# Kernel optimization log

Hardware: AMD Instinct MI355X
Metric: run time of the kernel (lower is better)

Reference implementation:

```python
import jax, jax.numpy as jnp
import numpy as np

B, L, H = 2, 2048, 2048
DI, N, DTR, K = 4096, 16, 128, 4  # intermediate, state, dt_rank, conv kernel


def setup_inputs() -> dict:
    key = jax.random.key(0)
    ks = jax.random.split(key, 8)
    x = jax.random.normal(ks[0], (B, L, H), jnp.float32)
    in_proj_w = jax.random.normal(ks[1], (2 * DI, H), jnp.float32) * 0.02
    conv1d_w = jax.random.normal(ks[2], (DI, 1, K), jnp.float32) * 0.1
    conv1d_b = jnp.zeros((DI,), jnp.float32)
    x_proj_w = jax.random.normal(ks[3], (DTR + 2 * N, DI), jnp.float32) * 0.02
    bound = DTR ** -0.5
    dt_proj_w = jax.random.uniform(ks[4], (DI, DTR), jnp.float32, -bound, bound)
    # faithful dt bias init: inverse-softplus of dt ~ Uniform-log[0.001, 0.1]
    dt = jnp.exp(jax.random.uniform(ks[5], (DI,), jnp.float32)
                 * (np.log(0.1) - np.log(0.001)) + np.log(0.001))
    dt = jnp.clip(dt, 1e-4)
    dt_proj_b = dt + jnp.log(-jnp.expm1(-dt))
    A_log = jnp.log(jnp.broadcast_to(jnp.arange(1, N + 1, dtype=jnp.float32), (DI, N)))
    D = jnp.ones((DI,), jnp.float32)
    out_proj_w = jax.random.normal(ks[6], (H, DI), jnp.float32) * 0.02
    return dict(x=x, in_proj_w=in_proj_w, conv1d_w=conv1d_w, conv1d_b=conv1d_b,
                x_proj_w=x_proj_w, dt_proj_w=dt_proj_w, dt_proj_b=dt_proj_b,
                A_log=A_log, D=D, out_proj_w=out_proj_w)


def _mamba_forward(x, in_proj_w, conv1d_w, conv1d_b, x_proj_w,
                   dt_proj_w, dt_proj_b, A_log, D, out_proj_w):
    # in_proj -> split into ssm input and gate (res)
    x_and_res = jnp.einsum('blh,eh->ble', x, in_proj_w)          # [B,L,2*DI]
    xi, res = jnp.split(x_and_res, 2, axis=-1)                    # [B,L,DI] each

    # depthwise causal conv1d (kernel K, left-pad K-1, truncated to L)
    xc = jnp.transpose(xi, (0, 2, 1))                             # [B,DI,L]
    xc = jax.lax.conv_general_dilated(
        xc, conv1d_w, window_strides=(1,), padding=((K - 1, 0),),
        dimension_numbers=('NCH', 'OIH', 'NCH'), feature_group_count=DI)
    xc = xc + conv1d_b[None, :, None]
    u = jax.nn.silu(jnp.transpose(xc, (0, 2, 1)))                 # [B,L,DI]

    # selective SSM parameters
    A = -jnp.exp(A_log.astype(jnp.float32))                       # [DI,N]
    x_dbl = jnp.einsum('bld,ed->ble', u, x_proj_w)                # [B,L,DTR+2N]
    dlt, Bm, Cm = jnp.split(x_dbl, [DTR, DTR + N], axis=-1)
    delta = jax.nn.softplus(jnp.einsum('blr,dr->bld', dlt, dt_proj_w) + dt_proj_b)

    # selective scan over time; carry h: [B,DI,N]
    def step(h, inp):
        d_t, B_t, C_t, u_t = inp                                  # [B,DI],[B,N],[B,N],[B,DI]
        dA = jnp.exp(d_t[:, :, None] * A)                         # [B,DI,N]
        h = dA * h + d_t[:, :, None] * B_t[:, None, :] * u_t[:, :, None]
        y_t = jnp.einsum('bdn,bn->bd', h, C_t)
        return h, y_t

    xs = (jnp.transpose(delta, (1, 0, 2)), jnp.transpose(Bm, (1, 0, 2)),
          jnp.transpose(Cm, (1, 0, 2)), jnp.transpose(u, (1, 0, 2)))
    h0 = jnp.zeros((x.shape[0], DI, N), jnp.float32)
    _, ys = jax.lax.scan(step, h0, xs)                            # ys: [L,B,DI]
    y = jnp.transpose(ys, (1, 0, 2)) + u * D.astype(jnp.float32)  # skip via D

    y = y * jax.nn.silu(res)                                      # gate
    return jnp.einsum('bld,hd->blh', y, out_proj_w)               # [B,L,H]


def reference(x, in_proj_w, conv1d_w, conv1d_b, x_proj_w,
              dt_proj_w, dt_proj_b, A_log, D, out_proj_w):
    return _mamba_forward(x, in_proj_w, conv1d_w, conv1d_b, x_proj_w,
                          dt_proj_w, dt_proj_b, A_log, D, out_proj_w)
```

## Files before the change

kernel.cpp:

```cpp
#include <hip/hip_runtime.h>
#include <hip/hip_bf16.h>
#include <stdint.h>

#define DEV static __device__ __forceinline__

typedef __attribute__((ext_vector_type(8))) short short8;
typedef __attribute__((ext_vector_type(4))) float f32x4;
typedef __attribute__((address_space(3))) void lds_void;
typedef __attribute__((address_space(1))) void glb_void;

constexpr int CB = 2, CL = 2048, CH = 2048, CDI = 4096, CN = 16, CDTR = 128;
constexpr int BLR = CB * CL;
constexpr int NC = 32, LC = 64;

DEV ushort f2b(float f) {
  union { float f; uint32_t u; } v; v.f = f;
  uint32_t u = v.u;
  return (ushort)((u + 0x7fffu + ((u >> 16) & 1u)) >> 16);
}
DEV float b2f(ushort b) {
  union { uint32_t u; float f; } v; v.u = ((uint32_t)b) << 16;
  return v.f;
}
DEV void gload16(const ushort* g, ushort* l) {
  __builtin_amdgcn_global_load_lds((const glb_void*)g, (lds_void*)l, 16, 0, 0);
}

__global__ void cast_kernel(const float* __restrict__ in, ushort* __restrict__ out, int n4) {
  int i = blockIdx.x * blockDim.x + threadIdx.x;
  if (i >= n4) return;
  float4 v = *(const float4*)(in + (size_t)i * 4);
  *(ushort4*)(out + (size_t)i * 4) = make_ushort4(f2b(v.x), f2b(v.y), f2b(v.z), f2b(v.w));
}

__global__ void cast_pad_xproj_kernel(const float* __restrict__ in, ushort* __restrict__ out) {
  int i = blockIdx.x * blockDim.x + threadIdx.x;
  if (i >= (256 * 4096 / 4)) return;
  int idx = i * 4;
  int r = idx >> 12;
  ushort4 o;
  if (r < 160) {
    float4 v = *(const float4*)(in + idx);
    o = make_ushort4(f2b(v.x), f2b(v.y), f2b(v.z), f2b(v.w));
  } else {
    o = make_ushort4(0, 0, 0, 0);
  }
  *(ushort4*)(out + idx) = o;
}

__global__ void dlt_cast_kernel(const float* __restrict__ xdbl, ushort* __restrict__ dlt) {
  int i = blockIdx.x * blockDim.x + threadIdx.x;
  if (i >= (BLR * CDTR / 4)) return;
  int idx = i * 4;
  int m = idx >> 7, c = idx & 127;
  float4 v = *(const float4*)(xdbl + (size_t)m * 256 + c);
  *(ushort4*)(dlt + idx) = make_ushort4(f2b(v.x), f2b(v.y), f2b(v.z), f2b(v.w));
}

__global__ void conv_silu_kernel(const ushort* __restrict__ xr, const float* __restrict__ w,
                                 const float* __restrict__ bias, ushort* __restrict__ u) {
  int t = blockIdx.x * blockDim.x + threadIdx.x;
  if (t >= BLR * CDI / 2) return;
  int d2 = t & (CDI / 2 - 1);
  int bl = t >> 11;
  int l = bl & (CL - 1);
  int d = d2 << 1;
  float4 w0 = *(const float4*)(w + (size_t)d * 4);
  float4 w1 = *(const float4*)(w + (size_t)d * 4 + 4);
  float wa0[4] = {w0.x, w0.y, w0.z, w0.w};
  float wa1[4] = {w1.x, w1.y, w1.z, w1.w};
  float a0 = bias[d], a1 = bias[d + 1];
#pragma unroll
  for (int k = 0; k < 4; ++k) {
    int ls = l - 3 + k;
    if (ls >= 0) {
      ushort2 xv = *(const ushort2*)(xr + (size_t)(bl - 3 + k) * 8192 + d);
      a0 = fmaf(wa0[k], b2f(xv.x), a0);
      a1 = fmaf(wa1[k], b2f(xv.y), a1);
    }
  }
  float s0 = a0 / (1.f + __expf(-a0));
  float s1 = a1 / (1.f + __expf(-a1));
  *(ushort2*)(u + (size_t)bl * 4096 + d) = make_ushort2(f2b(s0), f2b(s1));
}

template<int EPI>
__global__ __launch_bounds__(256, 2)
void gemm_bt_kernel(const ushort* __restrict__ A, const ushort* __restrict__ Bw,
                    void* __restrict__ Cp, const float* __restrict__ bias,
                    int M, int N, int K) {
  __shared__ ushort sA[128 * 32];
  __shared__ ushort sB[128 * 32];
  const int tid = threadIdx.x;
  const int bm = blockIdx.x, bn = blockIdx.y;
  const int w = tid >> 6, l = tid & 63;
  const int wr = w >> 1, wc = w & 1;
  const int q = l >> 4, r = l & 15;

  f32x4 acc[4][4] = {};

  const ushort* Ab = A + (size_t)bm * 128 * K;
  const ushort* Bb = Bw + (size_t)bn * 128 * K;
  const int nk = K >> 5;
  for (int kt = 0; kt < nk; ++kt) {
    const int k0 = kt << 5;
#pragma unroll
    for (int i = 0; i < 2; ++i) {
      const int chunk = i * 256 + tid;
      const int row = chunk >> 2;
      const int cofs = (chunk & 3) << 3;
      gload16(Ab + (size_t)row * K + k0 + cofs, sA + chunk * 8);
      gload16(Bb + (size_t)row * K + k0 + cofs, sB + chunk * 8);
    }
    __syncthreads();
    short8 af[4], bfg[4];
#pragma unroll
    for (int i = 0; i < 4; ++i) {
      af[i]  = *(const short8*)(sA + (wr * 64 + i * 16 + r) * 32 + q * 8);
      bfg[i] = *(const short8*)(sB + (wc * 64 + i * 16 + r) * 32 + q * 8);
    }
#pragma unroll
    for (int i = 0; i < 4; ++i)
#pragma unroll
      for (int j = 0; j < 4; ++j)
        acc[i][j] = __builtin_amdgcn_mfma_f32_16x16x32_bf16(af[i], bfg[j], acc[i][j], 0, 0, 0);
    __syncthreads();
  }

  const int m0 = bm * 128 + wr * 64;
  const int n0 = bn * 128 + wc * 64;
#pragma unroll
  for (int i = 0; i < 4; ++i) {
#pragma unroll
    for (int j = 0; j < 4; ++j) {
#pragma unroll
      for (int v = 0; v < 4; ++v) {
        const int grow = m0 + i * 16 + q * 4 + v;
        const int gcol = n0 + j * 16 + r;
        const float val = acc[i][j][v];
        if (EPI == 0) {
          ((ushort*)Cp)[(size_t)grow * N + gcol] = f2b(val);
        } else if (EPI == 1) {
          ((float*)Cp)[(size_t)grow * N + gcol] = val;
        } else {
          float xv = val + bias[gcol];
          float sp = xv > 20.f ? xv : log1pf(__expf(xv));
          ((ushort*)Cp)[(size_t)grow * N + gcol] = f2b(sp);
        }
      }
    }
  }
}

__global__ __launch_bounds__(256)
void scan_pass1_kernel(const ushort* __restrict__ delta_bf, const ushort* __restrict__ u_bf,
                       const float* __restrict__ xdbl, const float* __restrict__ A_log,
                       float* __restrict__ Hc, float* __restrict__ Ssum) {
  __shared__ float4 sB[LC * 4];
  const int blk = blockIdx.x;
  const int dblk = blk & 15, bc = blk >> 4;
  const int b = bc & (CB - 1), c = bc >> 1;
  const int tid = threadIdx.x;
  const int d = dblk * 256 + tid;
  const size_t rowbase = (size_t)b * CL + c * LC;

  {
    const int rr = tid >> 2, seg = tid & 3;
    sB[tid] = *(const float4*)(xdbl + (rowbase + rr) * 256 + 128 + seg * 4);
  }
  __syncthreads();

  float Ae[16];
#pragma unroll
  for (int n = 0; n < 16; ++n) Ae[n] = -__expf(A_log[(size_t)d * CN + n]);
  float h[16] = {};
  float S = 0.f;
  for (int t = 0; t < LC; ++t) {
    const float dl = b2f(delta_bf[(rowbase + t) * 4096 + d]);
    const float uu = b2f(u_bf[(rowbase + t) * 4096 + d]);
    const float du = dl * uu;
    S += dl;
#pragma unroll
    for (int q = 0; q < 4; ++q) {
      float4 bq = sB[t * 4 + q];
      h[q * 4 + 0] = __expf(Ae[q * 4 + 0] * dl) * h[q * 4 + 0] + du * bq.x;
      h[q * 4 + 1] = __expf(Ae[q * 4 + 1] * dl) * h[q * 4 + 1] + du * bq.y;
      h[q * 4 + 2] = __expf(Ae[q * 4 + 2] * dl) * h[q * 4 + 2] + du * bq.z;
      h[q * 4 + 3] = __expf(Ae[q * 4 + 3] * dl) * h[q * 4 + 3] + du * bq.w;
    }
  }
  float4* Hp = (float4*)(Hc + ((((size_t)c * CB + b) * CDI + d) << 4));
#pragma unroll
  for (int q = 0; q < 4; ++q)
    Hp[q] = make_float4(h[q * 4 + 0], h[q * 4 + 1], h[q * 4 + 2], h[q * 4 + 3]);
  Ssum[((size_t)c * CB + b) * CDI + d] = S;
}

__global__ __launch_bounds__(256)
void scan_pass2_kernel(float* __restrict__ Hc, const float* __restrict__ Ssum,
                       const float* __restrict__ A_log) {
  const int t = blockIdx.x * 256 + threadIdx.x;
  const int n = t & 15, d = (t >> 4) & (CDI - 1), b = t >> 16;
  const float Ae = -__expf(A_log[(size_t)d * CN + n]);
  float h = 0.f;
  for (int c = 1; c < NC; ++c) {
    const size_t idxp = ((size_t)(c - 1) * CB + b) * CDI + d;
    const float P = __expf(Ae * Ssum[idxp]);
    h = P * h + Hc[idxp * 16 + n];
    Hc[idxp * 16 + n] = h;
  }
}

__global__ __launch_bounds__(256)
void scan_pass3_kernel(const ushort* __restrict__ delta_bf, const ushort* __restrict__ u_bf,
                       const float* __restrict__ xdbl, const ushort* __restrict__ xr,
                       const float* __restrict__ A_log, const float* __restrict__ Dvec,
                       const float* __restrict__ Hc, ushort* __restrict__ ybf) {
  __shared__ float4 sB[LC * 4];
  __shared__ float4 sC[LC * 4];
  const int blk = blockIdx.x;
  const int dblk = blk & 15, bc = blk >> 4;
  const int b = bc & (CB - 1), c = bc >> 1;
  const int tid = threadIdx.x;
  const int d = dblk * 256 + tid;
  const size_t rowbase = (size_t)b * CL + c * LC;

  {
    const int rr = tid >> 2, seg = tid & 3;
    sB[tid] = *(const float4*)(xdbl + (rowbase + rr) * 256 + 128 + seg * 4);
    sC[tid] = *(const float4*)(xdbl + (rowbase + rr) * 256 + 144 + seg * 4);
  }
  __syncthreads();

  float Ae[16];
#pragma unroll
  for (int n = 0; n < 16; ++n) Ae[n] = -__expf(A_log[(size_t)d * CN + n]);
  float h[16];
  if (c == 0) {
#pragma unroll
    for (int n = 0; n < 16; ++n) h[n] = 0.f;
  } else {
    const float4* Hp = (const float4*)(Hc + ((((size_t)(c - 1) * CB + b) * CDI + d) << 4));
#pragma unroll
    for (int q = 0; q < 4; ++q) {
      float4 hv = Hp[q];
      h[q * 4 + 0] = hv.x; h[q * 4 + 1] = hv.y; h[q * 4 + 2] = hv.z; h[q * 4 + 3] = hv.w;
    }
  }
  const float Dd = Dvec[d];
  for (int t = 0; t < LC; ++t) {
    const float dl = b2f(delta_bf[(rowbase + t) * 4096 + d]);
    const float uu = b2f(u_bf[(rowbase + t) * 4096 + d]);
    const float du = dl * uu;
    float y = 0.f;
#pragma unroll
    for (int q = 0; q < 4; ++q) {
      float4 bq = sB[t * 4 + q];
      float4 cq = sC[t * 4 + q];
      h[q * 4 + 0] = __expf(Ae[q * 4 + 0] * dl) * h[q * 4 + 0] + du * bq.x;
      h[q * 4 + 1] = __expf(Ae[q * 4 + 1] * dl) * h[q * 4 + 1] + du * bq.y;
      h[q * 4 + 2] = __expf(Ae[q * 4 + 2] * dl) * h[q * 4 + 2] + du * bq.z;
      h[q * 4 + 3] = __expf(Ae[q * 4 + 3] * dl) * h[q * 4 + 3] + du * bq.w;
      y = fmaf(h[q * 4 + 0], cq.x, y);
      y = fmaf(h[q * 4 + 1], cq.y, y);
      y = fmaf(h[q * 4 + 2], cq.z, y);
      y = fmaf(h[q * 4 + 3], cq.w, y);
    }
    const float res = b2f(xr[(rowbase + t) * 8192 + 4096 + d]);
    const float sres = res / (1.f + __expf(-res));
    ybf[(rowbase + t) * 4096 + d] = f2b((y + uu * Dd) * sres);
  }
}

extern "C" void kernel_launch(void* const* d_in, const int* in_sizes, int n_in,
                              void* d_out, int out_size, void* d_ws, size_t ws_size,
                              hipStream_t stream) {
  (void)in_sizes; (void)n_in; (void)out_size; (void)ws_size;
  const float* x       = (const float*)d_in[0];
  const float* in_w    = (const float*)d_in[1];
  const float* conv_w  = (const float*)d_in[2];
  const float* conv_b  = (const float*)d_in[3];
  const float* xproj_w = (const float*)d_in[4];
  const float* dt_w    = (const float*)d_in[5];
  const float* dt_b    = (const float*)d_in[6];
  const float* A_log   = (const float*)d_in[7];
  const float* Dvec    = (const float*)d_in[8];
  const float* out_w   = (const float*)d_in[9];
  float* out = (float*)d_out;
  char* ws = (char*)d_ws;
  const size_t MB = 1u << 20;

  ushort* xb    = (ushort*)(ws);
  float*  Hc    = (float*)(ws);
  ushort* wout  = (ushort*)(ws);
  ushort* wb1   = (ushort*)(ws + 16 * MB);
  ushort* u_bf  = (ushort*)(ws + 16 * MB);
  ushort* xr    = (ushort*)(ws + 48 * MB);
  ushort* delta = (ushort*)(ws + 112 * MB);
  ushort* ybf   = (ushort*)(ws + 144 * MB);
  float*  xdbl  = (float*)(ws + 176 * MB);
  ushort* dlt   = (ushort*)(ws + 180 * MB);
  ushort* wxp   = (ushort*)(ws + 181 * MB);
  ushort* wdt   = (ushort*)(ws + 183 * MB);
  float*  Ssum  = (float*)(ws + 184 * MB);

  auto cast = [&](const float* in, ushort* o, int n) {
    cast_kernel<<<(n / 4 + 255) / 256, 256, 0, stream>>>(in, o, n / 4);
  };

  cast(x, xb, BLR * CH);
  cast(in_w, wb1, 2 * CDI * CH);
  gemm_bt_kernel<0><<<dim3(BLR / 128, (2 * CDI) / 128), 256, 0, stream>>>(
      xb, wb1, xr, nullptr, BLR, 2 * CDI, CH);
  conv_silu_kernel<<<(BLR * CDI / 2) / 256, 256, 0, stream>>>(xr, conv_w, conv_b, u_bf);
  cast_pad_xproj_kernel<<<(256 * 4096 / 4) / 256, 256, 0, stream>>>(xproj_w, wxp);
  gemm_bt_kernel<1><<<dim3(BLR / 128, 2), 256, 0, stream>>>(
      u_bf, wxp, xdbl, nullptr, BLR, 256, CDI);
  dlt_cast_kernel<<<(BLR * CDTR / 4) / 256, 256, 0, stream>>>(xdbl, dlt);
  cast(dt_w, wdt, CDI * CDTR);
  gemm_bt_kernel<2><<<dim3(BLR / 128, CDI / 128), 256, 0, stream>>>(
      dlt, wdt, delta, dt_b, BLR, CDI, CDTR);
  scan_pass1_kernel<<<NC * CB * (CDI / 256), 256, 0, stream>>>(
      delta, u_bf, xdbl, A_log, Hc, Ssum);
  scan_pass2_kernel<<<(CB * CDI * CN) / 256, 256, 0, stream>>>(Hc, Ssum, A_log);
  scan_pass3_kernel<<<NC * CB * (CDI / 256), 256, 0, stream>>>(
      delta, u_bf, xdbl, xr, A_log, Dvec, Hc, ybf);
  cast(out_w, wout, CH * CDI);
  gemm_bt_kernel<1><<<dim3(BLR / 128, CH / 128), 256, 0, stream>>>(
      ybf, wout, out, nullptr, BLR, CH, CDI);
}
```

Before: 627.3 us.

## Add 256-row tile GEMM with 4-stage async LDS pipeline for in/out projections

Adds a new 512-thread GEMM kernel using 256xBN block tiles, a 4-deep ring of direct-to-LDS global loads with explicit vmcnt waits, XOR-swizzled shared layout, and MFMA 16x16x32 bf16. The in_proj and out_proj GEMMs switch from the 128x128 kernel to this one, aiming for more operand reuse per block and loads overlapped with compute. In exchange it uses far more LDS and registers per block, so only one block fits per CU. Grid sizes shrink, which can leave CUs underused, especially for the out_proj GEMM.

```diff
diff --git a/kernel.cpp b/kernel.cpp
--- a/kernel.cpp
+++ b/kernel.cpp
@@ -150,6 +150,88 @@
       }
     }
   }
+}
+
+template<int NREP, int EPI>
+__global__ __launch_bounds__(512, 1)
+void gemm256_kernel(const ushort* __restrict__ A, const ushort* __restrict__ Bw,
+                    void* __restrict__ Cp, int N, int K) {
+  constexpr int BN = 64 * NREP;
+  constexpr int SBUFB = BN * 32;
+  __shared__ ushort sA[4 * 8192];
+  __shared__ ushort sB[4 * SBUFB];
+  const int tid = threadIdx.x;
+  const int bm = blockIdx.x, bn = blockIdx.y;
+  const int w = tid >> 6, l = tid & 63;
+  const int wr = w >> 2, wc = w & 3;
+  const int q = l >> 4, r = l & 15;
+
+  const ushort* Ab = A + (size_t)bm * 256 * K;
+  const ushort* Bb = Bw + (size_t)bn * BN * K;
+  const int c0 = tid, c1 = tid + 512;
+  const int ar0 = c0 >> 2, as0 = (c0 & 3) ^ ((ar0 >> 1) & 3);
+  const int ar1 = c1 >> 2, as1 = (c1 & 3) ^ ((ar1 >> 1) & 3);
+  const ushort* gA0 = Ab + (size_t)ar0 * K + as0 * 8;
+  const ushort* gA1 = Ab + (size_t)ar1 * K + as1 * 8;
+  const ushort* gB0 = Bb + (size_t)ar0 * K + as0 * 8;
+  const ushort* gB1 = Bb + (size_t)ar1 * K + as1 * 8;
+  const int nt = K >> 5;
+
+  auto stage = [&](int T) {
+    const int Tsrc = (T < nt) ? T : (nt - 1);
+    const int sl = T & 3;
+    const int ko = Tsrc << 5;
+    gload16(gA0 + ko, sA + sl * 8192 + c0 * 8);
+    gload16(gA1 + ko, sA + sl * 8192 + c1 * 8);
+    gload16(gB0 + ko, sB + sl * SBUFB + c0 * 8);
+    if constexpr (NREP == 4) gload16(gB1 + ko, sB + sl * SBUFB + c1 * 8);
+  };
+
+  const int soff = (q ^ ((r >> 1) & 3)) * 8;
+  const int aoff = (wr * 128 + r) * 32 + soff;
+  const int boff = (wc * 16 * NREP + r) * 32 + soff;
+
+  f32x4 acc[8][NREP] = {};
+
+  stage(0); stage(1); stage(2);
+  for (int t = 0; t < nt; ++t) {
+    stage(t + 3);
+    if constexpr (NREP == 4) asm volatile("s_waitcnt vmcnt(12)" ::: "memory");
+    else                     asm volatile("s_waitcnt vmcnt(9)" ::: "memory");
+    __builtin_amdgcn_s_barrier();
+    __builtin_amdgcn_sched_barrier(0);
+    const ushort* At = sA + (t & 3) * 8192 + aoff;
+    const ushort* Bt = sB + (t & 3) * SBUFB + boff;
+    short8 bfr[NREP];
+#pragma unroll
+    for (int n = 0; n < NREP; ++n) bfr[n] = *(const short8*)(Bt + n * 512);
+    __builtin_amdgcn_s_setprio(1);
+#pragma unroll
+    for (int m = 0; m < 8; ++m) {
+      short8 af = *(const short8*)(At + m * 512);
+#pragma unroll
+      for (int n = 0; n < NREP; ++n)
+        acc[m][n] = __builtin_amdgcn_mfma_f32_16x16x32_bf16(af, bfr[n], acc[m][n], 0, 0, 0);
+    }
+    __builtin_amdgcn_s_setprio(0);
+    __builtin_amdgcn_sched_barrier(0);
+    asm volatile("" ::: "memory");
+    __builtin_amdgcn_s_barrier();
+  }
+
+  const int m0g = bm * 256 + wr * 128;
+  const int n0g = bn * BN + wc * 16 * NREP;
+#pragma unroll
+  for (int m = 0; m < 8; ++m)
+#pragma unroll
+    for (int n = 0; n < NREP; ++n)
+#pragma unroll
+      for (int v = 0; v < 4; ++v) {
+        const int grow = m0g + m * 16 + q * 4 + v;
+        const int gcol = n0g + n * 16 + r;
+        if (EPI == 0) ((ushort*)Cp)[(size_t)grow * N + gcol] = f2b(acc[m][n][v]);
+        else          ((float*)Cp)[(size_t)grow * N + gcol]  = acc[m][n][v];
+      }
 }
 
 __global__ __launch_bounds__(256)
@@ -310,8 +392,8 @@
 
   cast(x, xb, BLR * CH);
   cast(in_w, wb1, 2 * CDI * CH);
-  gemm_bt_kernel<0><<<dim3(BLR / 128, (2 * CDI) / 128), 256, 0, stream>>>(
-      xb, wb1, xr, nullptr, BLR, 2 * CDI, CH);
+  gemm256_kernel<4, 0><<<dim3(BLR / 256, (2 * CDI) / 256), 512, 0, stream>>>(
+      xb, wb1, xr, 2 * CDI, CH);
   conv_silu_kernel<<<(BLR * CDI / 2) / 256, 256, 0, stream>>>(xr, conv_w, conv_b, u_bf);
   cast_pad_xproj_kernel<<<(256 * 4096 / 4) / 256, 256, 0, stream>>>(xproj_w, wxp);
   gemm_bt_kernel<1><<<dim3(BLR / 128, 2), 256, 0, stream>>>(
@@ -326,6 +408,6 @@
   scan_pass3_kernel<<<NC * CB * (CDI / 256), 256, 0, stream>>>(
       delta, u_bf, xdbl, xr, A_log, Dvec, Hc, ybf);
   cast(out_w, wout, CH * CDI);
-  gemm_bt_kernel<1><<<dim3(BLR / 128, CH / 128), 256, 0, stream>>>(
-      ybf, wout, out, nullptr, BLR, CH, CDI);
-}
+  gemm256_kernel<2, 1><<<dim3(BLR / 256, CH / 128), 512, 0, stream>>>(
+      ybf, wout, out, CH, CDI);
+}
```

After: 652.4 us. 4.0% more time.

## Split-K the x_proj GEMM and fuse reduction with delta cast

Applied to the files above, without the earlier changes.

The skinny x_proj GEMM (M=4096, N=256, K=4096) launched only 64 blocks. It is now split along K into 8 slices that write fp32 partials, followed by a reduce kernel that sums them, writes xdbl and emits the bf16 dt-rank slice, replacing the separate dlt cast kernel. The GEMM launch bounds are also raised to 4 blocks per SM to increase occupancy. The cost is extra partial-sum traffic of about 32 MB and a possible register-pressure penalty on the big GEMMs.

```diff
diff --git a/kernel.cpp b/kernel.cpp
--- a/kernel.cpp
+++ b/kernel.cpp
@@ -12,6 +12,7 @@
 constexpr int CB = 2, CL = 2048, CH = 2048, CDI = 4096, CN = 16, CDTR = 128;
 constexpr int BLR = CB * CL;
 constexpr int NC = 32, LC = 64;
+constexpr int KSL = 8;
 
 DEV ushort f2b(float f) {
   union { float f; uint32_t u; } v; v.f = f;
@@ -46,15 +47,6 @@
     o = make_ushort4(0, 0, 0, 0);
   }
   *(ushort4*)(out + idx) = o;
-}
-
-__global__ void dlt_cast_kernel(const float* __restrict__ xdbl, ushort* __restrict__ dlt) {
-  int i = blockIdx.x * blockDim.x + threadIdx.x;
-  if (i >= (BLR * CDTR / 4)) return;
-  int idx = i * 4;
-  int m = idx >> 7, c = idx & 127;
-  float4 v = *(const float4*)(xdbl + (size_t)m * 256 + c);
-  *(ushort4*)(dlt + idx) = make_ushort4(f2b(v.x), f2b(v.y), f2b(v.z), f2b(v.w));
 }
 
 __global__ void conv_silu_kernel(const ushort* __restrict__ xr, const float* __restrict__ w,
@@ -85,7 +77,7 @@
 }
 
 template<int EPI>
-__global__ __launch_bounds__(256, 2)
+__global__ __launch_bounds__(256, 4)
 void gemm_bt_kernel(const ushort* __restrict__ A, const ushort* __restrict__ Bw,
                     void* __restrict__ Cp, const float* __restrict__ bias,
                     int M, int N, int K) {
@@ -149,6 +141,78 @@
         }
       }
     }
+  }
+}
+
+__global__ __launch_bounds__(256, 4)
+void gemm_btk_kernel(const ushort* __restrict__ A, const ushort* __restrict__ Bw,
+                     float* __restrict__ Cpart, int N, int Ktot, int Ksl) {
+  __shared__ ushort sA[128 * 32];
+  __shared__ ushort sB[128 * 32];
+  const int tid = threadIdx.x;
+  const int bm = blockIdx.x, bn = blockIdx.y, z = blockIdx.z;
+  const int w = tid >> 6, l = tid & 63;
+  const int wr = w >> 1, wc = w & 1;
+  const int q = l >> 4, r = l & 15;
+
+  f32x4 acc[4][4] = {};
+
+  const ushort* Ab = A + (size_t)bm * 128 * Ktot + z * Ksl;
+  const ushort* Bb = Bw + (size_t)bn * 128 * Ktot + z * Ksl;
+  const int nk = Ksl >> 5;
+  for (int kt = 0; kt < nk; ++kt) {
+    const int k0 = kt << 5;
+#pragma unroll
+    for (int i = 0; i < 2; ++i) {
+      const int chunk = i * 256 + tid;
+      const int row = chunk >> 2;
+      const int cofs = (chunk & 3) << 3;
+      gload16(Ab + (size_t)row * Ktot + k0 + cofs, sA + chunk * 8);
+      gload16(Bb + (size_t)row * Ktot + k0 + cofs, sB + chunk * 8);
+    }
+    __syncthreads();
+    short8 af[4], bfg[4];
+#pragma unroll
+    for (int i = 0; i < 4; ++i) {
+      af[i]  = *(const short8*)(sA + (wr * 64 + i * 16 + r) * 32 + q * 8);
+      bfg[i] = *(const short8*)(sB + (wc * 64 + i * 16 + r) * 32 + q * 8);
+    }
+#pragma unroll
+    for (int i = 0; i < 4; ++i)
+#pragma unroll
+      for (int j = 0; j < 4; ++j)
+        acc[i][j] = __builtin_amdgcn_mfma_f32_16x16x32_bf16(af[i], bfg[j], acc[i][j], 0, 0, 0);
+    __syncthreads();
+  }
+
+  float* Cz = Cpart + (size_t)z * BLR * N;
+  const int m0 = bm * 128 + wr * 64;
+  const int n0 = bn * 128 + wc * 64;
+#pragma unroll
+  for (int i = 0; i < 4; ++i)
+#pragma unroll
+    for (int j = 0; j < 4; ++j)
+#pragma unroll
+      for (int v = 0; v < 4; ++v)
+        Cz[(size_t)(m0 + i * 16 + q * 4 + v) * N + (n0 + j * 16 + r)] = acc[i][j][v];
+}
+
+__global__ __launch_bounds__(256)
+void reduce_xdbl_kernel(const float* __restrict__ part, float* __restrict__ xdbl,
+                        ushort* __restrict__ dlt) {
+  const int i = blockIdx.x * 256 + threadIdx.x;
+  const int idx = i * 4;
+  const int row = idx >> 8, col = idx & 255;
+  float4 s = make_float4(0.f, 0.f, 0.f, 0.f);
+#pragma unroll
+  for (int z = 0; z < KSL; ++z) {
+    float4 v = *(const float4*)(part + (size_t)z * BLR * 256 + idx);
+    s.x += v.x; s.y += v.y; s.z += v.z; s.w += v.w;
+  }
+  *(float4*)(xdbl + idx) = s;
+  if (col < 128) {
+    *(ushort4*)(dlt + (size_t)row * 128 + col) =
+        make_ushort4(f2b(s.x), f2b(s.y), f2b(s.z), f2b(s.w));
   }
 }
 
@@ -296,6 +360,7 @@
   ushort* wb1   = (ushort*)(ws + 16 * MB);
   ushort* u_bf  = (ushort*)(ws + 16 * MB);
   ushort* xr    = (ushort*)(ws + 48 * MB);
+  float*  part  = (float*)(ws + 112 * MB);
   ushort* delta = (ushort*)(ws + 112 * MB);
   ushort* ybf   = (ushort*)(ws + 144 * MB);
   float*  xdbl  = (float*)(ws + 176 * MB);
@@ -314,9 +379,9 @@
       xb, wb1, xr, nullptr, BLR, 2 * CDI, CH);
   conv_silu_kernel<<<(BLR * CDI / 2) / 256, 256, 0, stream>>>(xr, conv_w, conv_b, u_bf);
   cast_pad_xproj_kernel<<<(256 * 4096 / 4) / 256, 256, 0, stream>>>(xproj_w, wxp);
-  gemm_bt_kernel<1><<<dim3(BLR / 128, 2), 256, 0, stream>>>(
-      u_bf, wxp, xdbl, nullptr, BLR, 256, CDI);
-  dlt_cast_kernel<<<(BLR * CDTR / 4) / 256, 256, 0, stream>>>(xdbl, dlt);
+  gemm_btk_kernel<<<dim3(BLR / 128, 2, KSL), 256, 0, stream>>>(
+      u_bf, wxp, part, 256, CDI, CDI / KSL);
+  reduce_xdbl_kernel<<<(BLR * 256 / 4) / 256, 256, 0, stream>>>(part, xdbl, dlt);
   cast(dt_w, wdt, CDI * CDTR);
   gemm_bt_kernel<2><<<dim3(BLR / 128, CDI / 128), 256, 0, stream>>>(
       dlt, wdt, delta, dt_b, BLR, CDI, CDTR);
```

Measured after the change: 583.8 us. -6.9%, faster.
